# Optimization experiments

Hardware: AMD Instinct MI355X
Metric: run time of the kernel (lower is better)

## Reference

```python
import jax, jax.numpy as jnp
import numpy as np

NW = 4096      # num_words in document
H = 768        # encoder hidden size
NC = 49152     # number of candidate spans
MSW = 30       # max_span_width
E = 20         # span width embedding size
M = 1024       # mlp hidden size
SPAN_EMB = 3 * H + E  # ment_emb='attn' -> start + end + attn term + width emb
NEG = -1e10


def setup_inputs() -> dict:
    key = jax.random.key(0)
    ks = jax.random.split(key, 16)
    s = 0.02
    encoded_doc = jax.random.normal(ks[0], (NW, H), jnp.float32)
    cand_starts = jax.random.randint(ks[1], (NC,), 0, NW - MSW)
    widths = jax.random.randint(ks[2], (NC,), 0, MSW)
    cand_ends = cand_starts + widths  # guaranteed < NW
    return {
        "encoded_doc": encoded_doc,
        "cand_starts": cand_starts,
        "cand_ends": cand_ends,
        "width_emb": jax.random.normal(ks[3], (MSW, E), jnp.float32) * s,
        "width_prior_emb": jax.random.normal(ks[4], (MSW, E), jnp.float32) * s,
        "attn_w": jax.random.normal(ks[5], (H,), jnp.float32) * s,
        "attn_b": jnp.zeros((1,), jnp.float32),
        "mlp1_w": jax.random.normal(ks[6], (SPAN_EMB, M), jnp.float32) * s,
        "mlp1_b": jnp.zeros((M,), jnp.float32),
        "mlp2_w": jax.random.normal(ks[7], (M,), jnp.float32) * s,
        "mlp2_b": jnp.zeros((1,), jnp.float32),
        "wmlp1_w": jax.random.normal(ks[8], (E, M), jnp.float32) * s,
        "wmlp1_b": jnp.zeros((M,), jnp.float32),
        "wmlp2_w": jax.random.normal(ks[9], (M,), jnp.float32) * s,
        "wmlp2_b": jnp.zeros((1,), jnp.float32),
    }


def reference(encoded_doc, cand_starts, cand_ends, width_emb, width_prior_emb,
              attn_w, attn_b, mlp1_w, mlp1_b, mlp2_w, mlp2_b,
              wmlp1_w, wmlp1_b, wmlp2_w, wmlp2_b):
    # span width index (clamped), shared by both width embedding tables
    width_idx = jnp.clip(cand_ends - cand_starts, 0, MSW - 1)

    # --- get_span_embeddings ---
    start_emb = encoded_doc[cand_starts]                 # [NC, H]
    end_emb = encoded_doc[cand_ends]                     # [NC, H]
    w_emb = width_emb[width_idx]                         # [NC, E]

    word_attn = encoded_doc @ attn_w + attn_b[0]         # [NW]
    doc_range = jnp.arange(NW)
    ment_mask = (doc_range[None, :] >= cand_starts[:, None]) & \
                (doc_range[None, :] <= cand_ends[:, None])       # [NC, NW]
    # original: (1 - mask)*-1e10 + word_attn
    scores = jnp.where(ment_mask, 0.0, NEG) + word_attn[None, :]
    mention_word_attn = jax.nn.softmax(scores, axis=1)   # [NC, NW]
    attention_term = mention_word_attn @ encoded_doc     # [NC, H]

    span_emb = jnp.concatenate([start_emb, end_emb, w_emb, attention_term],
                               axis=1)                   # [NC, 3H+E]

    # --- mention_mlp scoring (1 hidden ReLU layer -> scalar) ---
    h = jax.nn.relu(span_emb @ mlp1_w + mlp1_b)          # [NC, M]
    mention_logits = h @ mlp2_w + mlp2_b[0]              # [NC]

    # --- get_mention_width_scores ---
    wp = width_prior_emb[width_idx]                      # [NC, E]
    hw = jax.nn.relu(wp @ wmlp1_w + wmlp1_b)             # [NC, M]
    width_scores = hw @ wmlp2_w + wmlp2_b[0]             # [NC]

    return mention_logits + width_scores
```

## Files before the change

### kernel.cpp

```cpp
#include <hip/hip_runtime.h>
#include <math.h>

#define NW 4096
#define H 768
#define NC 49152
#define MSW 30
#define E 20
#define M 1024
#define CHUNK 64
#define NCH (NW / CHUNK)
#define NKT (H / 64)

typedef short bf16x8 __attribute__((ext_vector_type(8)));
typedef unsigned short u16x8 __attribute__((ext_vector_type(8)));
typedef float f32x4 __attribute__((ext_vector_type(4)));

__device__ __forceinline__ unsigned short f2bf(float x) {
    unsigned u = __float_as_uint(x);
    return (unsigned short)((u + 0x7fff + ((u >> 16) & 1)) >> 16);
}
__device__ __forceinline__ float bf2f(unsigned short b) {
    return __uint_as_float(((unsigned)b) << 16);
}
__device__ __forceinline__ void gload16(const void* g, void* l) {
    __builtin_amdgcn_global_load_lds((const __attribute__((address_space(1))) void*)g,
                                     (__attribute__((address_space(3))) void*)l, 16, 0, 0);
}

__global__ __launch_bounds__(256) void k_doc_prep(const float* __restrict__ doc,
                                                  const float* __restrict__ attn_w,
                                                  const float* __restrict__ attn_b,
                                                  unsigned short* __restrict__ docb,
                                                  float* __restrict__ ewa,
                                                  int* __restrict__ hist) {
    if (blockIdx.x < 16) hist[blockIdx.x * 256 + threadIdx.x] = 0;
    int row = blockIdx.x * 4 + (threadIdx.x >> 6);
    int lane = threadIdx.x & 63;
    const float* r = doc + (size_t)row * H;
    float s = 0.f;
    #pragma unroll
    for (int q = 0; q < 3; ++q) {
        int idx = q * 256 + lane * 4;
        float4 v = *reinterpret_cast<const float4*>(r + idx);
        float4 w = *reinterpret_cast<const float4*>(attn_w + idx);
        s += v.x * w.x + v.y * w.y + v.z * w.z + v.w * w.w;
        ushort4 o;
        o.x = f2bf(v.x); o.y = f2bf(v.y); o.z = f2bf(v.z); o.w = f2bf(v.w);
        *reinterpret_cast<ushort4*>(docb + (size_t)row * H + idx) = o;
    }
    #pragma unroll
    for (int off = 32; off > 0; off >>= 1) s += __shfl_down(s, off);
    if (lane == 0) ewa[row] = expf(s + attn_b[0]);
}

__global__ __launch_bounds__(256) void k_cvt_bt(const float* __restrict__ mlp1_w,
                                                unsigned short* __restrict__ Bt) {
    __shared__ float sh[32][33];
    int k0 = blockIdx.x * 32, m0 = blockIdx.y * 32, part = blockIdx.z;
    int rb = part == 0 ? 0 : (part == 1 ? H : (2 * H + E));
    int tx = threadIdx.x & 31, ty = threadIdx.x >> 5;
    #pragma unroll
    for (int it = 0; it < 4; ++it) {
        int kk = ty + it * 8;
        sh[kk][tx] = mlp1_w[(size_t)(rb + k0 + kk) * M + m0 + tx];
    }
    __syncthreads();
    #pragma unroll
    for (int it = 0; it < 4; ++it) {
        int mm = ty + it * 8;
        Bt[(size_t)(part * M + m0 + mm) * H + k0 + tx] = f2bf(sh[tx][mm]);
    }
}

__global__ __launch_bounds__(256) void k_scans2(const float* __restrict__ ewa,
                                                float* __restrict__ Dpre,
                                                const int* __restrict__ hist,
                                                int* __restrict__ offs,
                                                int* __restrict__ begs) {
    __shared__ float shf[256];
    __shared__ int shi[256];
    int t = threadIdx.x;
    if (blockIdx.x == 0) {
        float v[16];
        float sum = 0.f;
        #pragma unroll
        for (int i = 0; i < 16; ++i) { v[i] = ewa[t * 16 + i]; sum += v[i]; }
        shf[t] = sum;
        __syncthreads();
        for (int off = 1; off < 256; off <<= 1) {
            float x = (t >= off) ? shf[t - off] : 0.f;
            __syncthreads();
            shf[t] += x;
            __syncthreads();
        }
        float run = shf[t] - sum;
        #pragma unroll
        for (int i = 0; i < 16; ++i) { run += v[i]; Dpre[t * 16 + i + 1] = run; }
        if (t == 0) Dpre[0] = 0.f;
    } else {
        int v[16];
        int sum = 0;
        #pragma unroll
        for (int i = 0; i < 16; ++i) { v[i] = hist[t * 16 + i]; sum += v[i]; }
        shi[t] = sum;
        __syncthreads();
        for (int off = 1; off < 256; off <<= 1) {
            int x = (t >= off) ? shi[t - off] : 0;
            __syncthreads();
            shi[t] += x;
            __syncthreads();
        }
        int run = shi[t] - sum;
        #pragma unroll
        for (int i = 0; i < 16; ++i) {
            offs[t * 16 + i] = run;
            begs[t * 16 + i] = run;
            run += v[i];
        }
        if (t == 255) begs[4096] = run;
    }
}

__global__ __launch_bounds__(256) void k_pw_ws(const float* __restrict__ width_emb,
                                               const float* __restrict__ mlp1_w,
                                               const float* __restrict__ mlp1_b,
                                               float* __restrict__ PW,
                                               const float* __restrict__ wp_emb,
                                               const float* __restrict__ w1,
                                               const float* __restrict__ b1,
                                               const float* __restrict__ w2,
                                               const float* __restrict__ b2,
                                               float* __restrict__ wscore) {
    __shared__ float red[256];
    int w = blockIdx.x;
    int y = blockIdx.y;
    int tid = threadIdx.x;
    if (y < 4) {
        int m = y * 256 + tid;
        float acc = mlp1_b[m];
        #pragma unroll
        for (int e = 0; e < E; ++e)
            acc += width_emb[w * E + e] * mlp1_w[(size_t)(2 * H + e) * M + m];
        PW[w * M + m] = acc;
    } else {
        float part = 0.f;
        for (int m = tid; m < M; m += 256) {
            float h = b1[m];
            #pragma unroll
            for (int e = 0; e < E; ++e) h += wp_emb[w * E + e] * w1[e * M + m];
            part += fmaxf(h, 0.f) * w2[m];
        }
        red[tid] = part;
        __syncthreads();
        for (int s = 128; s > 0; s >>= 1) {
            if (tid < s) red[tid] += red[tid + s];
            __syncthreads();
        }
        if (tid == 0) wscore[w] = red[0] + b2[0];
    }
}

__global__ __launch_bounds__(256) void k_hist(const int* __restrict__ starts,
                                              int* __restrict__ hist) {
    atomicAdd(&hist[starts[blockIdx.x * 256 + threadIdx.x]], 1);
}
__global__ __launch_bounds__(256) void k_scatter(const int* __restrict__ starts,
                                                 int* __restrict__ offs,
                                                 int* __restrict__ perm) {
    int c = blockIdx.x * 256 + threadIdx.x;
    int p = atomicAdd(&offs[starts[c]], 1);
    perm[p] = c;
}

__global__ __launch_bounds__(512, 2) void k_proj_mfma(const unsigned short* __restrict__ docb,
                                                      const unsigned short* __restrict__ Bt,
                                                      const float* __restrict__ ewa,
                                                      unsigned short* __restrict__ Pse,
                                                      float* __restrict__ Sbuf,
                                                      float* __restrict__ T) {
    __shared__ unsigned short As[2][16384];
    __shared__ unsigned short Bs[2][12288];
    int tid = threadIdx.x;
    int bid = blockIdx.x;
    int xcd = bid & 7, rr0 = bid >> 3;
    int coltile = (xcd & 1) * 8 + (rr0 & 7);
    int rowtile = (xcd >> 1) * 4 + (rr0 >> 3);
    int col0 = coltile * 192;
    int row0 = rowtile * 256;
    int wv = tid >> 6, lane = tid & 63;
    int wr = wv >> 2, wc = wv & 3;

    f32x4 acc[8][3];
    #pragma unroll
    for (int mi = 0; mi < 8; ++mi)
        #pragma unroll
        for (int ni = 0; ni < 3; ++ni) acc[mi][ni] = (f32x4){0.f, 0.f, 0.f, 0.f};

    #define STAGE(buf, k0)                                                            \
        {                                                                             \
            _Pragma("unroll")                                                         \
            for (int i = 0; i < 4; ++i) {                                             \
                int s = i * 512 + tid;                                                \
                int mg = s >> 7, ks = (s >> 6) & 1, g = (s >> 4) & 3, ri = s & 15;    \
                gload16(docb + (size_t)(row0 + mg * 16 + ri) * H + (k0) + ks * 32 + g * 8, \
                        (char*)As[buf] + s * 16);                                     \
            }                                                                         \
            _Pragma("unroll")                                                         \
            for (int i = 0; i < 3; ++i) {                                             \
                int s = i * 512 + tid;                                                \
                int cg = s >> 7, ks = (s >> 6) & 1, g = (s >> 4) & 3, ci = s & 15;    \
                gload16(Bt + (size_t)(col0 + cg * 16 + ci) * H + (k0) + ks * 32 + g * 8, \
                        (char*)Bs[buf] + s * 16);                                     \
            }                                                                         \
        }

    STAGE(0, 0);
    STAGE(1, 64);
    asm volatile("s_waitcnt vmcnt(7)" ::: "memory");
    __builtin_amdgcn_s_barrier();

    #pragma unroll 1
    for (int t = 0; t < NKT; ++t) {
        int cur = t & 1;
        bf16x8 af[2][8], bfr[2][3];
        #pragma unroll
        for (int ks = 0; ks < 2; ++ks) {
            #pragma unroll
            for (int mi = 0; mi < 8; ++mi)
                af[ks][mi] = *reinterpret_cast<const bf16x8*>(
                    (char*)As[cur] + (wr * 8 + mi) * 2048 + ks * 1024 + lane * 16);
            #pragma unroll
            for (int ni = 0; ni < 3; ++ni)
                bfr[ks][ni] = *reinterpret_cast<const bf16x8*>(
                    (char*)Bs[cur] + (wc * 3 + ni) * 2048 + ks * 1024 + lane * 16);
        }
        __builtin_amdgcn_s_setprio(1);
        #pragma unroll
        for (int ks = 0; ks < 2; ++ks)
            #pragma unroll
            for (int mi = 0; mi < 8; ++mi)
                #pragma unroll
                for (int ni = 0; ni < 3; ++ni)
                    acc[mi][ni] = __builtin_amdgcn_mfma_f32_16x16x32_bf16(
                        af[ks][mi], bfr[ks][ni], acc[mi][ni], 0, 0, 0);
        __builtin_amdgcn_s_setprio(0);
        if (t + 2 < NKT) {
            asm volatile("s_waitcnt lgkmcnt(0)" ::: "memory");
            __builtin_amdgcn_sched_barrier(0);
            __builtin_amdgcn_s_barrier();
            STAGE(cur, (t + 2) * 64);
            asm volatile("s_waitcnt vmcnt(7)" ::: "memory");
            __builtin_amdgcn_s_barrier();
        } else if (t + 2 == NKT) {
            asm volatile("s_waitcnt vmcnt(0)" ::: "memory");
            __builtin_amdgcn_s_barrier();
        }
    }
    #undef STAGE

    int cr = (lane >> 4) * 4;
    int cc = lane & 15;
    #pragma unroll
    for (int mi = 0; mi < 8; ++mi) {
        #pragma unroll
        for (int ni = 0; ni < 3; ++ni) {
            int rrow = row0 + wr * 128 + mi * 16 + cr;
            int cabs = col0 + wc * 48 + ni * 16 + cc;
            int part = cabs >> 10;
            int cm = cabs & 1023;
            if (part < 2) {
                unsigned short* dst = Pse + (size_t)rrow * 2048 + part * 1024 + cm;
                #pragma unroll
                for (int j = 0; j < 4; ++j) dst[(size_t)j * 2048] = f2bf(acc[mi][ni][j]);
            } else {
                float* dst = Sbuf + (size_t)rrow * M + cm;
                #pragma unroll
                for (int j = 0; j < 4; ++j) dst[(size_t)j * M] = acc[mi][ni][j];
            }
        }
    }
    #pragma unroll
    for (int half = 0; half < 2; ++half) {
        int chunk = (row0 >> 6) + wr * 2 + half;
        #pragma unroll
        for (int ni = 0; ni < 3; ++ni) {
            int cabs = col0 + wc * 48 + ni * 16 + cc;
            if (cabs >= 2048) {
                float psum = 0.f;
                #pragma unroll
                for (int mi4 = 0; mi4 < 4; ++mi4) {
                    int mi = half * 4 + mi4;
                    int rbase = row0 + wr * 128 + mi * 16 + cr;
                    #pragma unroll
                    for (int j = 0; j < 4; ++j)
                        psum += ewa[rbase + j] * acc[mi][ni][j];
                }
                psum += __shfl_down(psum, 16);
                psum += __shfl_down(psum, 32);
                if ((lane >> 4) == 0)
                    T[(size_t)chunk * M + (cabs - 2048)] = psum;
            }
        }
    }
}

__global__ __launch_bounds__(256) void k_scan2(float* __restrict__ T) {
    int m = blockIdx.x * 256 + threadIdx.x;
    float v[NCH];
    #pragma unroll
    for (int c = 0; c < NCH; ++c) v[c] = T[c * M + m];
    float run = 0.f;
    #pragma unroll
    for (int c = 0; c < NCH; ++c) { float t = v[c]; T[c * M + m] = run; run += t; }
}

__global__ __launch_bounds__(256) void k_scan3(float* __restrict__ Sbuf,
                                               const float* __restrict__ ewa,
                                               const float* __restrict__ T) {
    int m = blockIdx.x * 256 + threadIdx.x;
    int c = blockIdx.y;
    __shared__ float ew[CHUNK];
    if (threadIdx.x < CHUNK) ew[threadIdx.x] = ewa[c * CHUNK + threadIdx.x];
    __syncthreads();
    float acc = T[c * M + m];
    float* base = Sbuf + (size_t)(c * CHUNK) * M + m;
    #pragma unroll 4
    for (int i = 0; i < CHUNK; ++i) {
        float* p = base + (size_t)i * M;
        acc += ew[i] * (*p);
        *p = acc;
    }
}

__global__ __launch_bounds__(256) void k_cand(const unsigned short* __restrict__ Pse,
                                              const float* __restrict__ Sbuf,
                                              const float* __restrict__ PW,
                                              const float* __restrict__ Dpre,
                                              const float* __restrict__ wscore,
                                              const int* __restrict__ perm,
                                              const int* __restrict__ begs,
                                              const int* __restrict__ ends,
                                              const float* __restrict__ mlp2_w,
                                              const float* __restrict__ mlp2_b,
                                              float* __restrict__ out) {
    __shared__ __align__(16) unsigned short ps_l[1024];
    __shared__ __align__(16) float ss_l[1024];
    int bid = blockIdx.x;
    int s = (bid & 7) * 512 + (bid >> 3);
    int tid = threadIdx.x;
    {
        ushort4 p4 = *reinterpret_cast<const ushort4*>(Pse + (size_t)s * 2048 + tid * 4);
        *reinterpret_cast<ushort4*>(ps_l + tid * 4) = p4;
        float4 s4 = (s > 0) ? *reinterpret_cast<const float4*>(Sbuf + (size_t)(s - 1) * M + tid * 4)
                            : make_float4(0.f, 0.f, 0.f, 0.f);
        *reinterpret_cast<float4*>(ss_l + tid * 4) = s4;
    }
    __syncthreads();
    int beg = begs[s], end = begs[s + 1];
    int wv = tid >> 6, lane = tid & 63;
    float dps = Dpre[s];

    for (int j = beg + wv; j < end; j += 4) {
        int c = perm[j];
        int e = ends[c];
        int wi = e - s;
        wi = wi > MSW - 1 ? MSW - 1 : wi;
        float inv = 1.f / (Dpre[e + 1] - dps);
        const unsigned short* pe = Pse + (size_t)e * 2048 + 1024;
        const float* se = Sbuf + (size_t)e * M;
        const float* pw = PW + (size_t)wi * M;

        float part = 0.f;
        #pragma unroll
        for (int q = 0; q < 2; ++q) {
            int m = lane * 8 + q * 512;
            u16x8 a8 = *reinterpret_cast<const u16x8*>(ps_l + m);
            u16x8 b8 = *reinterpret_cast<const u16x8*>(pe + m);
            float4 t0 = *reinterpret_cast<const float4*>(se + m);
            float4 t1 = *reinterpret_cast<const float4*>(se + m + 4);
            float4 u0 = *reinterpret_cast<const float4*>(ss_l + m);
            float4 u1 = *reinterpret_cast<const float4*>(ss_l + m + 4);
            float4 w0 = *reinterpret_cast<const float4*>(pw + m);
            float4 w1 = *reinterpret_cast<const float4*>(pw + m + 4);
            float4 v0 = *reinterpret_cast<const float4*>(mlp2_w + m);
            float4 v1 = *reinterpret_cast<const float4*>(mlp2_w + m + 4);
            float x;
            x = bf2f(a8[0]) + bf2f(b8[0]) + w0.x + (t0.x - u0.x) * inv; part += fmaxf(x, 0.f) * v0.x;
            x = bf2f(a8[1]) + bf2f(b8[1]) + w0.y + (t0.y - u0.y) * inv; part += fmaxf(x, 0.f) * v0.y;
            x = bf2f(a8[2]) + bf2f(b8[2]) + w0.z + (t0.z - u0.z) * inv; part += fmaxf(x, 0.f) * v0.z;
            x = bf2f(a8[3]) + bf2f(b8[3]) + w0.w + (t0.w - u0.w) * inv; part += fmaxf(x, 0.f) * v0.w;
            x = bf2f(a8[4]) + bf2f(b8[4]) + w1.x + (t1.x - u1.x) * inv; part += fmaxf(x, 0.f) * v1.x;
            x = bf2f(a8[5]) + bf2f(b8[5]) + w1.y + (t1.y - u1.y) * inv; part += fmaxf(x, 0.f) * v1.y;
            x = bf2f(a8[6]) + bf2f(b8[6]) + w1.z + (t1.z - u1.z) * inv; part += fmaxf(x, 0.f) * v1.z;
            x = bf2f(a8[7]) + bf2f(b8[7]) + w1.w + (t1.w - u1.w) * inv; part += fmaxf(x, 0.f) * v1.w;
        }
        #pragma unroll
        for (int off = 32; off > 0; off >>= 1) part += __shfl_down(part, off);
        if (lane == 0) out[c] = part + mlp2_b[0] + wscore[wi];
    }
}

extern "C" void kernel_launch(void* const* d_in, const int* in_sizes, int n_in,
                              void* d_out, int out_size, void* d_ws, size_t ws_size,
                              hipStream_t stream) {
    const float* encoded_doc = (const float*)d_in[0];
    const int*   cand_starts = (const int*)d_in[1];
    const int*   cand_ends   = (const int*)d_in[2];
    const float* width_emb   = (const float*)d_in[3];
    const float* width_prior = (const float*)d_in[4];
    const float* attn_w      = (const float*)d_in[5];
    const float* attn_b      = (const float*)d_in[6];
    const float* mlp1_w      = (const float*)d_in[7];
    const float* mlp1_b      = (const float*)d_in[8];
    const float* mlp2_w      = (const float*)d_in[9];
    const float* mlp2_b      = (const float*)d_in[10];
    const float* wmlp1_w     = (const float*)d_in[11];
    const float* wmlp1_b     = (const float*)d_in[12];
    const float* wmlp2_w     = (const float*)d_in[13];
    const float* wmlp2_b     = (const float*)d_in[14];
    float* out = (float*)d_out;

    float* Sbuf   = (float*)d_ws;
    float* T      = Sbuf + (size_t)NW * M;
    float* PW     = T + NCH * M;
    float* ewa    = PW + MSW * M;
    float* Dpre   = ewa + NW;
    float* wscore = Dpre + 4160;
    unsigned short* Pse  = (unsigned short*)(wscore + 64);
    unsigned short* docb = Pse + (size_t)NW * 2048;
    unsigned short* Btb  = docb + (size_t)NW * H;
    int* hist = (int*)(Btb + (size_t)3072 * H);
    int* offs = hist + 4096;
    int* begs = offs + 4096;
    int* perm = begs + 4112;

    k_doc_prep<<<NW / 4, 256, 0, stream>>>(encoded_doc, attn_w, attn_b, docb, ewa, hist);
    k_cvt_bt<<<dim3(H / 32, M / 32, 3), 256, 0, stream>>>(mlp1_w, Btb);
    k_hist<<<NC / 256, 256, 0, stream>>>(cand_starts, hist);
    k_scans2<<<2, 256, 0, stream>>>(ewa, Dpre, hist, offs, begs);
    k_pw_ws<<<dim3(MSW, 5), 256, 0, stream>>>(width_emb, mlp1_w, mlp1_b, PW,
                                              width_prior, wmlp1_w, wmlp1_b,
                                              wmlp2_w, wmlp2_b, wscore);
    k_scatter<<<NC / 256, 256, 0, stream>>>(cand_starts, offs, perm);
    k_proj_mfma<<<256, 512, 0, stream>>>(docb, Btb, ewa, Pse, Sbuf, T);
    k_scan2<<<M / 256, 256, 0, stream>>>(T);
    k_scan3<<<dim3(M / 256, NCH), 256, 0, stream>>>(Sbuf, ewa, T);
    k_cand<<<4096, 256, 0, stream>>>(Pse, Sbuf, PW, Dpre, wscore, perm, begs,
                                     cand_ends, mlp2_w, mlp2_b, out);
}
```

Measured before the change: 116.2 us.

## Fuse prep kernels, halve GEMM row tile, drop chunk scan kernel

```diff
diff --git a/kernel.cpp b/kernel.cpp
--- a/kernel.cpp
+++ b/kernel.cpp
@@ -27,48 +27,90 @@
                                      (__attribute__((address_space(3))) void*)l, 16, 0, 0);
 }
 
-__global__ __launch_bounds__(256) void k_doc_prep(const float* __restrict__ doc,
-                                                  const float* __restrict__ attn_w,
-                                                  const float* __restrict__ attn_b,
-                                                  unsigned short* __restrict__ docb,
-                                                  float* __restrict__ ewa,
-                                                  int* __restrict__ hist) {
-    if (blockIdx.x < 16) hist[blockIdx.x * 256 + threadIdx.x] = 0;
-    int row = blockIdx.x * 4 + (threadIdx.x >> 6);
-    int lane = threadIdx.x & 63;
-    const float* r = doc + (size_t)row * H;
-    float s = 0.f;
-    #pragma unroll
-    for (int q = 0; q < 3; ++q) {
-        int idx = q * 256 + lane * 4;
-        float4 v = *reinterpret_cast<const float4*>(r + idx);
-        float4 w = *reinterpret_cast<const float4*>(attn_w + idx);
-        s += v.x * w.x + v.y * w.y + v.z * w.z + v.w * w.w;
-        ushort4 o;
-        o.x = f2bf(v.x); o.y = f2bf(v.y); o.z = f2bf(v.z); o.w = f2bf(v.w);
-        *reinterpret_cast<ushort4*>(docb + (size_t)row * H + idx) = o;
-    }
-    #pragma unroll
-    for (int off = 32; off > 0; off >>= 1) s += __shfl_down(s, off);
-    if (lane == 0) ewa[row] = expf(s + attn_b[0]);
-}
-
-__global__ __launch_bounds__(256) void k_cvt_bt(const float* __restrict__ mlp1_w,
-                                                unsigned short* __restrict__ Bt) {
+__global__ __launch_bounds__(256) void k_prep(const float* __restrict__ doc,
+                                              const float* __restrict__ attn_w,
+                                              const float* __restrict__ attn_b,
+                                              unsigned short* __restrict__ docb,
+                                              float* __restrict__ ewa,
+                                              int* __restrict__ hist,
+                                              const float* __restrict__ mlp1_w,
+                                              unsigned short* __restrict__ Bt,
+                                              const float* __restrict__ width_emb,
+                                              const float* __restrict__ mlp1_b,
+                                              float* __restrict__ PW,
+                                              const float* __restrict__ wp_emb,
+                                              const float* __restrict__ w1,
+                                              const float* __restrict__ b1,
+                                              const float* __restrict__ w2,
+                                              const float* __restrict__ b2,
+                                              float* __restrict__ wscore) {
     __shared__ float sh[32][33];
-    int k0 = blockIdx.x * 32, m0 = blockIdx.y * 32, part = blockIdx.z;
-    int rb = part == 0 ? 0 : (part == 1 ? H : (2 * H + E));
-    int tx = threadIdx.x & 31, ty = threadIdx.x >> 5;
-    #pragma unroll
-    for (int it = 0; it < 4; ++it) {
-        int kk = ty + it * 8;
-        sh[kk][tx] = mlp1_w[(size_t)(rb + k0 + kk) * M + m0 + tx];
-    }
-    __syncthreads();
-    #pragma unroll
-    for (int it = 0; it < 4; ++it) {
-        int mm = ty + it * 8;
-        Bt[(size_t)(part * M + m0 + mm) * H + k0 + tx] = f2bf(sh[tx][mm]);
+    __shared__ float red[256];
+    int bx = blockIdx.x;
+    int tid = threadIdx.x;
+    if (bx < 1024) {
+        if (bx < 16) hist[bx * 256 + tid] = 0;
+        int row = bx * 4 + (tid >> 6);
+        int lane = tid & 63;
+        const float* r = doc + (size_t)row * H;
+        float s = 0.f;
+        #pragma unroll
+        for (int q = 0; q < 3; ++q) {
+            int idx = q * 256 + lane * 4;
+            float4 v = *reinterpret_cast<const float4*>(r + idx);
+            float4 w = *reinterpret_cast<const float4*>(attn_w + idx);
+            s += v.x * w.x + v.y * w.y + v.z * w.z + v.w * w.w;
+            ushort4 o;
+            o.x = f2bf(v.x); o.y = f2bf(v.y); o.z = f2bf(v.z); o.w = f2bf(v.w);
+            *reinterpret_cast<ushort4*>(docb + (size_t)row * H + idx) = o;
+        }
+        #pragma unroll
+        for (int off = 32; off > 0; off >>= 1) s += __shfl_down(s, off);
+        if (lane == 0) ewa[row] = expf(s + attn_b[0]);
+    } else if (bx < 3328) {
+        int idx = bx - 1024;
+        int k0 = (idx % 24) * 32;
+        int m0 = ((idx / 24) % 32) * 32;
+        int part = idx / (24 * 32);
+        int rb = part == 0 ? 0 : (part == 1 ? H : (2 * H + E));
+        int tx = tid & 31, ty = tid >> 5;
+        #pragma unroll
+        for (int it = 0; it < 4; ++it) {
+            int kk = ty + it * 8;
+            sh[kk][tx] = mlp1_w[(size_t)(rb + k0 + kk) * M + m0 + tx];
+        }
+        __syncthreads();
+        #pragma unroll
+        for (int it = 0; it < 4; ++it) {
+            int mm = ty + it * 8;
+            Bt[(size_t)(part * M + m0 + mm) * H + k0 + tx] = f2bf(sh[tx][mm]);
+        }
+    } else {
+        int idx = bx - 3328;
+        int w = idx / 5, y = idx % 5;
+        if (y < 4) {
+            int m = y * 256 + tid;
+            float acc = mlp1_b[m];
+            #pragma unroll
+            for (int e = 0; e < E; ++e)
+                acc += width_emb[w * E + e] * mlp1_w[(size_t)(2 * H + e) * M + m];
+            PW[w * M + m] = acc;
+        } else {
+            float part = 0.f;
+            for (int m = tid; m < M; m += 256) {
+                float h = b1[m];
+                #pragma unroll
+                for (int e = 0; e < E; ++e) h += wp_emb[w * E + e] * w1[e * M + m];
+                part += fmaxf(h, 0.f) * w2[m];
+            }
+            red[tid] = part;
+            __syncthreads();
+            for (int s = 128; s > 0; s >>= 1) {
+                if (tid < s) red[tid] += red[tid + s];
+                __syncthreads();
+            }
+            if (tid == 0) wscore[w] = red[0] + b2[0];
+        }
     }
 }
 
@@ -121,45 +163,6 @@
     }
 }
 
-__global__ __launch_bounds__(256) void k_pw_ws(const float* __restrict__ width_emb,
-                                               const float* __restrict__ mlp1_w,
-                                               const float* __restrict__ mlp1_b,
-                                               float* __restrict__ PW,
-                                               const float* __restrict__ wp_emb,
-                                               const float* __restrict__ w1,
-                                               const float* __restrict__ b1,
-                                               const float* __restrict__ w2,
-                                               const float* __restrict__ b2,
-                                               float* __restrict__ wscore) {
-    __shared__ float red[256];
-    int w = blockIdx.x;
-    int y = blockIdx.y;
-    int tid = threadIdx.x;
-    if (y < 4) {
-        int m = y * 256 + tid;
-        float acc = mlp1_b[m];
-        #pragma unroll
-        for (int e = 0; e < E; ++e)
-            acc += width_emb[w * E + e] * mlp1_w[(size_t)(2 * H + e) * M + m];
-        PW[w * M + m] = acc;
-    } else {
-        float part = 0.f;
-        for (int m = tid; m < M; m += 256) {
-            float h = b1[m];
-            #pragma unroll
-            for (int e = 0; e < E; ++e) h += wp_emb[w * E + e] * w1[e * M + m];
-            part += fmaxf(h, 0.f) * w2[m];
-        }
-        red[tid] = part;
-        __syncthreads();
-        for (int s = 128; s > 0; s >>= 1) {
-            if (tid < s) red[tid] += red[tid + s];
-            __syncthreads();
-        }
-        if (tid == 0) wscore[w] = red[0] + b2[0];
-    }
-}
-
 __global__ __launch_bounds__(256) void k_hist(const int* __restrict__ starts,
                                               int* __restrict__ hist) {
     atomicAdd(&hist[starts[blockIdx.x * 256 + threadIdx.x]], 1);
@@ -172,34 +175,34 @@
     perm[p] = c;
 }
 
-__global__ __launch_bounds__(512, 2) void k_proj_mfma(const unsigned short* __restrict__ docb,
+__global__ __launch_bounds__(512, 4) void k_proj_mfma(const unsigned short* __restrict__ docb,
                                                       const unsigned short* __restrict__ Bt,
                                                       const float* __restrict__ ewa,
                                                       unsigned short* __restrict__ Pse,
                                                       float* __restrict__ Sbuf,
                                                       float* __restrict__ T) {
-    __shared__ unsigned short As[2][16384];
+    __shared__ unsigned short As[2][8192];
     __shared__ unsigned short Bs[2][12288];
     int tid = threadIdx.x;
     int bid = blockIdx.x;
     int xcd = bid & 7, rr0 = bid >> 3;
     int coltile = (xcd & 1) * 8 + (rr0 & 7);
-    int rowtile = (xcd >> 1) * 4 + (rr0 >> 3);
+    int rowtile = (xcd >> 1) * 8 + (rr0 >> 3);
     int col0 = coltile * 192;
-    int row0 = rowtile * 256;
+    int row0 = rowtile * 128;
     int wv = tid >> 6, lane = tid & 63;
     int wr = wv >> 2, wc = wv & 3;
 
-    f32x4 acc[8][3];
+    f32x4 acc[4][3];
     #pragma unroll
-    for (int mi = 0; mi < 8; ++mi)
+    for (int mi = 0; mi < 4; ++mi)
         #pragma unroll
         for (int ni = 0; ni < 3; ++ni) acc[mi][ni] = (f32x4){0.f, 0.f, 0.f, 0.f};
 
     #define STAGE(buf, k0)                                                            \
         {                                                                             \
             _Pragma("unroll")                                                         \
-            for (int i = 0; i < 4; ++i) {                                             \
+            for (int i = 0; i < 2; ++i) {                                             \
                 int s = i * 512 + tid;                                                \
                 int mg = s >> 7, ks = (s >> 6) & 1, g = (s >> 4) & 3, ri = s & 15;    \
                 gload16(docb + (size_t)(row0 + mg * 16 + ri) * H + (k0) + ks * 32 + g * 8, \
@@ -216,40 +219,38 @@
 
     STAGE(0, 0);
     STAGE(1, 64);
-    asm volatile("s_waitcnt vmcnt(7)" ::: "memory");
+    asm volatile("s_waitcnt vmcnt(5)" ::: "memory");
     __builtin_amdgcn_s_barrier();
 
     #pragma unroll 1
     for (int t = 0; t < NKT; ++t) {
         int cur = t & 1;
-        bf16x8 af[2][8], bfr[2][3];
         #pragma unroll
         for (int ks = 0; ks < 2; ++ks) {
+            bf16x8 af[4], bfr[3];
             #pragma unroll
-            for (int mi = 0; mi < 8; ++mi)
-                af[ks][mi] = *reinterpret_cast<const bf16x8*>(
-                    (char*)As[cur] + (wr * 8 + mi) * 2048 + ks * 1024 + lane * 16);
+            for (int mi = 0; mi < 4; ++mi)
+                af[mi] = *reinterpret_cast<const bf16x8*>(
+                    (char*)As[cur] + (wr * 4 + mi) * 2048 + ks * 1024 + lane * 16);
             #pragma unroll
             for (int ni = 0; ni < 3; ++ni)
-                bfr[ks][ni] = *reinterpret_cast<const bf16x8*>(
+                bfr[ni] = *reinterpret_cast<const bf16x8*>(
                     (char*)Bs[cur] + (wc * 3 + ni) * 2048 + ks * 1024 + lane * 16);
-        }
-        __builtin_amdgcn_s_setprio(1);
-        #pragma unroll
-        for (int ks = 0; ks < 2; ++ks)
+            __builtin_amdgcn_s_setprio(1);
             #pragma unroll
-            for (int mi = 0; mi < 8; ++mi)
+            for (int mi = 0; mi < 4; ++mi)
                 #pragma unroll
                 for (int ni = 0; ni < 3; ++ni)
                     acc[mi][ni] = __builtin_amdgcn_mfma_f32_16x16x32_bf16(
-                        af[ks][mi], bfr[ks][ni], acc[mi][ni], 0, 0, 0);
-        __builtin_amdgcn_s_setprio(0);
+                        af[mi], bfr[ni], acc[mi][ni], 0, 0, 0);
+            __builtin_amdgcn_s_setprio(0);
+        }
         if (t + 2 < NKT) {
             asm volatile("s_waitcnt lgkmcnt(0)" ::: "memory");
             __builtin_amdgcn_sched_barrier(0);
             __builtin_amdgcn_s_barrier();
             STAGE(cur, (t + 2) * 64);
-            asm volatile("s_waitcnt vmcnt(7)" ::: "memory");
+            asm volatile("s_waitcnt vmcnt(5)" ::: "memory");
             __builtin_amdgcn_s_barrier();
         } else if (t + 2 == NKT) {
             asm volatile("s_waitcnt vmcnt(0)" ::: "memory");
@@ -261,10 +262,10 @@
     int cr = (lane >> 4) * 4;
     int cc = lane & 15;
     #pragma unroll
-    for (int mi = 0; mi < 8; ++mi) {
+    for (int mi = 0; mi < 4; ++mi) {
         #pragma unroll
         for (int ni = 0; ni < 3; ++ni) {
-            int rrow = row0 + wr * 128 + mi * 16 + cr;
+            int rrow = row0 + wr * 64 + mi * 16 + cr;
             int cabs = col0 + wc * 48 + ni * 16 + cc;
             int part = cabs >> 10;
             int cm = cabs & 1023;
@@ -279,18 +280,16 @@
             }
         }
     }
-    #pragma unroll
-    for (int half = 0; half < 2; ++half) {
-        int chunk = (row0 >> 6) + wr * 2 + half;
+    {
+        int chunk = (row0 >> 6) + wr;
         #pragma unroll
         for (int ni = 0; ni < 3; ++ni) {
             int cabs = col0 + wc * 48 + ni * 16 + cc;
             if (cabs >= 2048) {
                 float psum = 0.f;
                 #pragma unroll
-                for (int mi4 = 0; mi4 < 4; ++mi4) {
-                    int mi = half * 4 + mi4;
-                    int rbase = row0 + wr * 128 + mi * 16 + cr;
+                for (int mi = 0; mi < 4; ++mi) {
+                    int rbase = row0 + wr * 64 + mi * 16 + cr;
                     #pragma unroll
                     for (int j = 0; j < 4; ++j)
                         psum += ewa[rbase + j] * acc[mi][ni][j];
@@ -304,16 +303,6 @@
     }
 }
 
-__global__ __launch_bounds__(256) void k_scan2(float* __restrict__ T) {
-    int m = blockIdx.x * 256 + threadIdx.x;
-    float v[NCH];
-    #pragma unroll
-    for (int c = 0; c < NCH; ++c) v[c] = T[c * M + m];
-    float run = 0.f;
-    #pragma unroll
-    for (int c = 0; c < NCH; ++c) { float t = v[c]; T[c * M + m] = run; run += t; }
-}
-
 __global__ __launch_bounds__(256) void k_scan3(float* __restrict__ Sbuf,
                                                const float* __restrict__ ewa,
                                                const float* __restrict__ T) {
@@ -322,7 +311,8 @@
     __shared__ float ew[CHUNK];
     if (threadIdx.x < CHUNK) ew[threadIdx.x] = ewa[c * CHUNK + threadIdx.x];
     __syncthreads();
-    float acc = T[c * M + m];
+    float acc = 0.f;
+    for (int cp = 0; cp < c; ++cp) acc += T[(size_t)cp * M + m];
     float* base = Sbuf + (size_t)(c * CHUNK) * M + m;
     #pragma unroll 4
     for (int i = 0; i < CHUNK; ++i) {
@@ -359,6 +349,10 @@
     int beg = begs[s], end = begs[s + 1];
     int wv = tid >> 6, lane = tid & 63;
     float dps = Dpre[s];
+    float4 v00 = *reinterpret_cast<const float4*>(mlp2_w + lane * 8);
+    float4 v01 = *reinterpret_cast<const float4*>(mlp2_w + lane * 8 + 4);
+    float4 v10 = *reinterpret_cast<const float4*>(mlp2_w + lane * 8 + 512);
+    float4 v11 = *reinterpret_cast<const float4*>(mlp2_w + lane * 8 + 516);
 
     for (int j = beg + wv; j < end; j += 4) {
         int c = perm[j];
@@ -382,8 +376,8 @@
             float4 u1 = *reinterpret_cast<const float4*>(ss_l + m + 4);
             float4 w0 = *reinterpret_cast<const float4*>(pw + m);
             float4 w1 = *reinterpret_cast<const float4*>(pw + m + 4);
-            float4 v0 = *reinterpret_cast<const float4*>(mlp2_w + m);
-            float4 v1 = *reinterpret_cast<const float4*>(mlp2_w + m + 4);
+            float4 v0 = q ? v10 : v00;
+            float4 v1 = q ? v11 : v01;
             float x;
             x = bf2f(a8[0]) + bf2f(b8[0]) + w0.x + (t0.x - u0.x) * inv; part += fmaxf(x, 0.f) * v0.x;
             x = bf2f(a8[1]) + bf2f(b8[1]) + w0.y + (t0.y - u0.y) * inv; part += fmaxf(x, 0.f) * v0.y;
@@ -434,16 +428,13 @@
     int* begs = offs + 4096;
     int* perm = begs + 4112;
 
-    k_doc_prep<<<NW / 4, 256, 0, stream>>>(encoded_doc, attn_w, attn_b, docb, ewa, hist);
-    k_cvt_bt<<<dim3(H / 32, M / 32, 3), 256, 0, stream>>>(mlp1_w, Btb);
+    k_prep<<<3478, 256, 0, stream>>>(encoded_doc, attn_w, attn_b, docb, ewa, hist,
+                                     mlp1_w, Btb, width_emb, mlp1_b, PW,
+                                     width_prior, wmlp1_w, wmlp1_b, wmlp2_w, wmlp2_b, wscore);
     k_hist<<<NC / 256, 256, 0, stream>>>(cand_starts, hist);
     k_scans2<<<2, 256, 0, stream>>>(ewa, Dpre, hist, offs, begs);
-    k_pw_ws<<<dim3(MSW, 5), 256, 0, stream>>>(width_emb, mlp1_w, mlp1_b, PW,
-                                              width_prior, wmlp1_w, wmlp1_b,
-                                              wmlp2_w, wmlp2_b, wscore);
     k_scatter<<<NC / 256, 256, 0, stream>>>(cand_starts, offs, perm);
-    k_proj_mfma<<<256, 512, 0, stream>>>(docb, Btb, ewa, Pse, Sbuf, T);
-    k_scan2<<<M / 256, 256, 0, stream>>>(T);
+    k_proj_mfma<<<512, 512, 0, stream>>>(docb, Btb, ewa, Pse, Sbuf, T);
     k_scan3<<<dim3(M / 256, NCH), 256, 0, stream>>>(Sbuf, ewa, T);
     k_cand<<<4096, 256, 0, stream>>>(Pse, Sbuf, PW, Dpre, wscore, perm, begs,
                                      cand_ends, mlp2_w, mlp2_b, out);
```

Measured after the change: 119.4 us. +2.8%, slower.
